# Optimization experiments

Hardware: AMD Instinct MI355X
Metric: run time of the kernel (lower is better)

## Reference

```python
import jax, jax.numpy as jnp
import numpy as np

D_MODEL = 1024
N_HEADS = 16
D_K = D_MODEL // N_HEADS
MAX_LEN = 2048
B, T = 2, 2048


def setup_inputs() -> dict:
    key = jax.random.key(0)
    ks = jax.random.split(key, 10)
    s = 1.0 / np.sqrt(D_MODEL)
    inp = {
        "x": jax.random.normal(ks[0], (B, T, D_MODEL), dtype=jnp.float32),
        "WQ": jax.random.uniform(ks[1], (D_MODEL, D_MODEL), minval=-s, maxval=s, dtype=jnp.float32),
        "bQ": jax.random.uniform(ks[2], (D_MODEL,), minval=-s, maxval=s, dtype=jnp.float32),
        "WK": jax.random.uniform(ks[3], (D_MODEL, D_MODEL), minval=-s, maxval=s, dtype=jnp.float32),
        "bK": jax.random.uniform(ks[4], (D_MODEL,), minval=-s, maxval=s, dtype=jnp.float32),
        "WV": jax.random.uniform(ks[5], (D_MODEL, D_MODEL), minval=-s, maxval=s, dtype=jnp.float32),
        "bV": jax.random.uniform(ks[6], (D_MODEL,), minval=-s, maxval=s, dtype=jnp.float32),
        "WO": jax.random.uniform(ks[7], (D_MODEL, D_MODEL), minval=-s, maxval=s, dtype=jnp.float32),
        "bO": jax.random.uniform(ks[8], (D_MODEL,), minval=-s, maxval=s, dtype=jnp.float32),
        "rel_pos_table": jax.random.normal(ks[9], (2 * MAX_LEN - 1, N_HEADS), dtype=jnp.float32),
    }
    return inp


def reference(x, WQ, bQ, WK, bK, WV, bV, WO, bO, rel_pos_table):
    b, t, d = x.shape
    # torch Linear: y = x @ W^T + b
    q = (x @ WQ.T + bQ).reshape(b, t, N_HEADS, D_K).transpose(0, 2, 1, 3)  # [B,H,T,dk]
    k = (x @ WK.T + bK).reshape(b, t, N_HEADS, D_K).transpose(0, 2, 1, 3)
    v = (x @ WV.T + bV).reshape(b, t, N_HEADS, D_K).transpose(0, 2, 1, 3)

    scores = jnp.einsum("bhqd,bhkd->bhqk", q, k) / jnp.sqrt(jnp.float32(D_K))

    pos = jnp.arange(t)
    rel = pos[:, None] - pos[None, :] + (MAX_LEN - 1)
    rel = jnp.clip(rel, 0, 2 * MAX_LEN - 2)
    rel_bias = rel_pos_table[rel]                  # [T,T,H]
    scores = scores + rel_bias.transpose(2, 0, 1)[None]  # [1,H,T,T]

    causal = pos[None, :] <= pos[:, None]          # [T,T] lower-triangular
    scores = jnp.where(causal[None, None], scores, -jnp.inf)

    attn = jax.nn.softmax(scores, axis=-1)
    out = jnp.einsum("bhqk,bhkd->bhqd", attn, v)   # [B,H,T,dk]
    out = out.transpose(0, 2, 1, 3).reshape(b, t, d)
    return out @ WO.T + bO
```

## Files before the change

### kernel.cpp

```cpp
#include <hip/hip_runtime.h>
#include <hip/hip_bf16.h>

typedef __attribute__((ext_vector_type(8))) short bf16x8;
typedef __attribute__((ext_vector_type(4))) float f32x4;
typedef __attribute__((ext_vector_type(16))) float f32x16;

#define MFMA16(a, b, c) __builtin_amdgcn_mfma_f32_16x16x32_bf16(a, b, c, 0, 0, 0)
#define MFMA32(a, b, c) __builtin_amdgcn_mfma_f32_32x32x16_bf16(a, b, c, 0, 0, 0)

__device__ inline ushort f2b(float f) {
  union { float f; unsigned u; } v; v.f = f;
  unsigned u = v.u;
  u += 0x7fffu + ((u >> 16) & 1u);
  return (ushort)(u >> 16);
}

__device__ inline unsigned cvtpk(float lo, float hi) {
  unsigned r;
  asm("v_cvt_pk_bf16_f32 %0, %1, %2" : "=v"(r) : "v"(lo), "v"(hi));
  return r;
}

__device__ inline void plswap(unsigned& a, unsigned& b) {
  asm("v_permlane32_swap_b32 %0, %1" : "+v"(a), "+v"(b));
}

__global__ void cast_k(const float* __restrict__ in, ushort* __restrict__ out, int n) {
  int i = (blockIdx.x * blockDim.x + threadIdx.x) * 4;
  const int stride = gridDim.x * blockDim.x * 4;
  for (; i < n; i += stride) {
    float4 v = *reinterpret_cast<const float4*>(in + i);
    ushort4 o;
    o.x = f2b(v.x); o.y = f2b(v.y); o.z = f2b(v.z); o.w = f2b(v.w);
    *reinterpret_cast<ushort4*>(out + i) = o;
  }
}

__global__ void cast_w(const float* __restrict__ wq, const float* __restrict__ wk,
                       const float* __restrict__ wv, const float* __restrict__ wo,
                       ushort* __restrict__ wcat, ushort* __restrict__ wob) {
  const int i = (blockIdx.x * 256 + threadIdx.x) * 4;
  const int which = i >> 20, off = i & 1048575;
  const float* src = (which == 0) ? wq : (which == 1) ? wk : (which == 2) ? wv : wo;
  float4 v = *reinterpret_cast<const float4*>(src + off);
  ushort4 o;
  o.x = f2b(v.x); o.y = f2b(v.y); o.z = f2b(v.z); o.w = f2b(v.w);
  if (which < 3) *reinterpret_cast<ushort4*>(wcat + i) = o;
  else           *reinterpret_cast<ushort4*>(wob + off) = o;
}

__global__ void prep_rel(const float* __restrict__ relT, float* __restrict__ relvT) {
  const int t = blockIdx.x * 256 + threadIdx.x;
  if (t >= 16 * 4095) return;
  const int h = t / 4095, d = t - h * 4095;
  relvT[t] = relT[(size_t)d * 16 + h] * 1.4426950408889634f;
}

__global__ __launch_bounds__(256, 4)
void repack_kv(const ushort* __restrict__ Kg, const ushort* __restrict__ VTg,
               ushort* __restrict__ Kf, ushort* __restrict__ Vf) {
  const int blk = blockIdx.x;
  const int bh = blk >> 5, t64 = blk & 31;
  const int tid = threadIdx.x;
  const int w = tid >> 6, lane = tid & 63;
  const int li = lane & 31, hi = lane >> 5;
  const size_t dstbase = (size_t)blk * 4096 + lane * 8;
  const int half = w & 1;
  if (w < 2) {
#pragma unroll
    for (int c = 0; c < 4; ++c) {
      bf16x8 v = *reinterpret_cast<const bf16x8*>(
          Kg + ((size_t)(bh * 2048 + t64 * 64 + half * 32 + li)) * 64 + c * 16 + hi * 8);
      *reinterpret_cast<bf16x8*>(Kf + dstbase + (half * 4 + c) * 512) = v;
    }
  } else {
#pragma unroll
    for (int c = 0; c < 4; ++c) {
      bf16x8 v = *reinterpret_cast<const bf16x8*>(
          VTg + ((size_t)(bh * 64 + half * 32 + li)) * 2048 + t64 * 64 + c * 16 + hi * 8);
      *reinterpret_cast<bf16x8*>(Vf + dstbase + (half * 4 + c) * 512) = v;
    }
  }
}

template <int MODE>
__global__ __launch_bounds__(256, 3)
void gemm_bt(const ushort* __restrict__ A, const ushort* __restrict__ B,
             const float* __restrict__ b0, const float* __restrict__ b1,
             const float* __restrict__ b2,
             float* __restrict__ outF, ushort* __restrict__ Qg,
             ushort* __restrict__ Kg, ushort* __restrict__ VTg, int N) {
  __shared__ __align__(16) ushort As[128][32];
  __shared__ __align__(16) ushort Bs[128][32];
  const int tid = threadIdx.x;
  const int m0 = blockIdx.y * 128, n0 = blockIdx.x * 128;
  const int wid = tid >> 6, lane = tid & 63, g = lane >> 4, li = lane & 15;
  const int wr = (wid >> 1) * 64, wc = (wid & 1) * 64;
  const int srow = lane >> 2, scol = (lane & 3) * 8;
  const ushort* gA0 = A + (size_t)(m0 + wid * 32 + srow) * 1024 + scol;
  const ushort* gB0 = B + (size_t)(n0 + wid * 32 + srow) * 1024 + scol;
  ushort* lA0 = &As[wid * 32][0];
  ushort* lA1 = &As[wid * 32 + 16][0];
  ushort* lB0 = &Bs[wid * 32][0];
  ushort* lB1 = &Bs[wid * 32 + 16][0];
  f32x4 acc[4][4] = {};
  for (int k0 = 0; k0 < 1024; k0 += 32) {
    __builtin_amdgcn_global_load_lds((const __attribute__((address_space(1))) void*)(gA0 + k0),
                                     (__attribute__((address_space(3))) void*)lA0, 16, 0, 0);
    __builtin_amdgcn_global_load_lds((const __attribute__((address_space(1))) void*)(gA0 + 16 * 1024 + k0),
                                     (__attribute__((address_space(3))) void*)lA1, 16, 0, 0);
    __builtin_amdgcn_global_load_lds((const __attribute__((address_space(1))) void*)(gB0 + k0),
                                     (__attribute__((address_space(3))) void*)lB0, 16, 0, 0);
    __builtin_amdgcn_global_load_lds((const __attribute__((address_space(1))) void*)(gB0 + 16 * 1024 + k0),
                                     (__attribute__((address_space(3))) void*)lB1, 16, 0, 0);
    __syncthreads();
    bf16x8 af[4], bfm[4];
#pragma unroll
    for (int i = 0; i < 4; ++i) {
      af[i]  = *reinterpret_cast<const bf16x8*>(&As[wr + i * 16 + li][g * 8]);
      bfm[i] = *reinterpret_cast<const bf16x8*>(&Bs[wc + i * 16 + li][g * 8]);
    }
#pragma unroll
    for (int mi = 0; mi < 4; ++mi)
#pragma unroll
      for (int ni = 0; ni < 4; ++ni)
        acc[mi][ni] = MFMA16(af[mi], bfm[ni], acc[mi][ni]);
    __syncthreads();
  }
#pragma unroll
  for (int mi = 0; mi < 4; ++mi) {
#pragma unroll
    for (int ni = 0; ni < 4; ++ni) {
      const int col = n0 + wc + ni * 16 + li;
      if (MODE == 0) {
#pragma unroll
        for (int r = 0; r < 4; ++r) {
          const int row = m0 + wr + mi * 16 + 4 * g + r;
          outF[(size_t)row * N + col] = acc[mi][ni][r] + b0[col];
        }
      } else {
        const int which = col >> 10, c = col & 1023;
        const int hh = c >> 6, dk = c & 63;
        const float* bias = (which == 0) ? b0 : ((which == 1) ? b1 : b2);
        const float bcol = bias[c];
        const int row0 = m0 + wr + mi * 16 + 4 * g;
        const int bb = row0 >> 11, t0 = row0 & 2047;
        const size_t bhi = (size_t)(bb * 16 + hh);
        if (which == 2) {
          ushort4 o;
          o.x = f2b(acc[mi][ni][0] + bcol);
          o.y = f2b(acc[mi][ni][1] + bcol);
          o.z = f2b(acc[mi][ni][2] + bcol);
          o.w = f2b(acc[mi][ni][3] + bcol);
          *reinterpret_cast<ushort4*>(VTg + (bhi * 64 + dk) * 2048 + t0) = o;
        } else {
          ushort* dst = ((which == 0) ? Qg : Kg) + (bhi * 2048 + t0) * 64 + dk;
#pragma unroll
          for (int r = 0; r < 4; ++r)
            dst[(size_t)r * 64] = f2b(acc[mi][ni][r] + bcol);
        }
      }
    }
  }
}

__device__ __forceinline__ void attn_phase(
    const int qt, const int wid, const int lane, const int li, const int hi,
    const int h, const int bb,
    const ushort* __restrict__ Qb, const ushort* __restrict__ Kfb,
    const ushort* __restrict__ Vfb, const float* relv,
    float Obuf[3][64][33], float lbuf[3][64], ushort* __restrict__ Oa) {
  const int q = qt * 32 + li;
  bf16x8 qf[4];
#pragma unroll
  for (int c = 0; c < 4; ++c)
    qf[c] = *reinterpret_cast<const bf16x8*>(Qb + (size_t)q * 64 + c * 16 + hi * 8);
  f32x16 O[2] = {};
  float lacc[4] = {0.f, 0.f, 0.f, 0.f};
  const int nkt = (qt >> 1) + 1;
  const int nt = (wid < nkt) ? ((nkt - 1 - wid) >> 2) + 1 : 0;
  const int mask_kb = (nkt - 1) * 64;
  const float C1 = 0.18033688f;
  for (int i = 0; i < nt; ++i) {
    const int kb = wid * 64 + i * 256;
    const ushort* Kt = Kfb + (size_t)(kb >> 6) * 4096 + lane * 8;
    const ushort* Vt = Vfb + (size_t)(kb >> 6) * 4096 + lane * 8;
    bf16x8 Kr[8], Vr[8];
#pragma unroll
    for (int j = 0; j < 8; ++j)
      Kr[j] = *reinterpret_cast<const bf16x8*>(Kt + j * 512);
#pragma unroll
    for (int j = 0; j < 8; ++j)
      Vr[j] = *reinterpret_cast<const bf16x8*>(Vt + j * 512);
    __builtin_amdgcn_sched_barrier(0);
    f32x16 S0 = {}, S1 = {};
#pragma unroll
    for (int c = 0; c < 4; ++c) S0 = MFMA32(Kr[c], qf[c], S0);
#pragma unroll
    for (int c = 0; c < 4; ++c) S1 = MFMA32(Kr[4 + c], qf[c], S1);
    const int dqb = q - kb - 4 * hi;
    const float* rl = relv + (dqb - 63);
    if (kb != mask_kb) {
#pragma unroll
      for (int r = 0; r < 16; ++r) {
        const int off0 = (r & 3) + 8 * (r >> 2);
        const float p0 = __builtin_amdgcn_exp2f(fmaf(S0[r], C1, rl[63 - off0]));
        const float p1 = __builtin_amdgcn_exp2f(fmaf(S1[r], C1, rl[31 - off0]));
        S0[r] = p0; S1[r] = p1;
        lacc[r & 3] += p0 + p1;
      }
    } else {
#pragma unroll
      for (int r = 0; r < 16; ++r) {
        const int off0 = (r & 3) + 8 * (r >> 2);
        const int d0 = dqb - off0, d1 = d0 - 32;
        float p0 = __builtin_amdgcn_exp2f(fmaf(S0[r], C1, relv[d0 & 2047]));
        float p1 = __builtin_amdgcn_exp2f(fmaf(S1[r], C1, relv[d1 & 2047]));
        p0 = (d0 >= 0) ? p0 : 0.f;
        p1 = (d1 >= 0) ? p1 : 0.f;
        S0[r] = p0; S1[r] = p1;
        lacc[r & 3] += p0 + p1;
      }
    }
    unsigned U0[4][2], U1[4][2];
#pragma unroll
    for (int rg = 0; rg < 4; ++rg) {
      U0[rg][0] = cvtpk(S0[4 * rg + 0], S0[4 * rg + 1]);
      U0[rg][1] = cvtpk(S0[4 * rg + 2], S0[4 * rg + 3]);
      U1[rg][0] = cvtpk(S1[4 * rg + 0], S1[4 * rg + 1]);
      U1[rg][1] = cvtpk(S1[4 * rg + 2], S1[4 * rg + 3]);
    }
#pragma unroll
    for (int c = 0; c < 4; ++c) {
      const int c0 = c & 1;
      unsigned x0 = (c < 2) ? U0[2 * c0][0] : U1[2 * c0][0];
      unsigned y0 = (c < 2) ? U0[2 * c0 + 1][0] : U1[2 * c0 + 1][0];
      unsigned x1 = (c < 2) ? U0[2 * c0][1] : U1[2 * c0][1];
      unsigned y1 = (c < 2) ? U0[2 * c0 + 1][1] : U1[2 * c0 + 1][1];
      plswap(x0, y0);
      plswap(x1, y1);
      union { unsigned u[4]; bf16x8 v; } P;
      P.u[0] = x0; P.u[1] = x1; P.u[2] = y0; P.u[3] = y1;
#pragma unroll
      for (int db = 0; db < 2; ++db)
        O[db] = MFMA32(Vr[db * 4 + c], P.v, O[db]);
    }
  }
  __syncthreads();
  if (wid) {
    float* ob = &Obuf[wid - 1][lane][0];
#pragma unroll
    for (int db = 0; db < 2; ++db)
#pragma unroll
      for (int r = 0; r < 16; ++r)
        ob[db * 16 + r] = O[db][r];
    lbuf[wid - 1][lane] = lacc[0] + lacc[1] + lacc[2] + lacc[3];
  }
  __syncthreads();
  if (wid == 0) {
    float lh = lacc[0] + lacc[1] + lacc[2] + lacc[3];
#pragma unroll
    for (int w = 0; w < 3; ++w) {
      lh += lbuf[w][lane];
      const float* ob = &Obuf[w][lane][0];
#pragma unroll
      for (int db = 0; db < 2; ++db)
#pragma unroll
        for (int r = 0; r < 16; ++r)
          O[db][r] += ob[db * 16 + r];
    }
    unsigned xa = __float_as_uint(lh), xb2 = xa;
    plswap(xa, xb2);
    const float linv = 1.f / (__uint_as_float(xa) + __uint_as_float(xb2));
    ushort* orow = Oa + ((size_t)(bb * 2048 + q)) * 1024 + h * 64;
#pragma unroll
    for (int db = 0; db < 2; ++db)
#pragma unroll
      for (int rg = 0; rg < 4; ++rg) {
        ushort4 o;
        o.x = f2b(O[db][4 * rg + 0] * linv);
        o.y = f2b(O[db][4 * rg + 1] * linv);
        o.z = f2b(O[db][4 * rg + 2] * linv);
        o.w = f2b(O[db][4 * rg + 3] * linv);
        *reinterpret_cast<ushort4*>(orow + db * 32 + 8 * rg + 4 * hi) = o;
      }
  }
}

__global__ __launch_bounds__(256, 2)
void attn_k(const ushort* __restrict__ Qg, const ushort* __restrict__ Kf,
            const ushort* __restrict__ Vf, const float* __restrict__ relvT,
            ushort* __restrict__ Oa) {
  __shared__ float relv[2048];
  __shared__ float Obuf[3][64][33];
  __shared__ float lbuf[3][64];
  const int f = blockIdx.x;
  const int bh = (f & 7) * 4 + (f >> 8);
  const int qp = (f >> 3) & 31;
  const int h = bh & 15, bb = bh >> 4;
  {
    const float* src = relvT + h * 4095 + 2047;
    for (int i = threadIdx.x; i < 2048; i += 256) relv[i] = src[i];
  }
  __syncthreads();
  const int wid = threadIdx.x >> 6, lane = threadIdx.x & 63;
  const int li = lane & 31, hi = lane >> 5;
  const ushort* Qb  = Qg + (size_t)bh * (2048 * 64);
  const ushort* Kfb = Kf + (size_t)bh * (32 * 4096);
  const ushort* Vfb = Vf + (size_t)bh * (32 * 4096);
  attn_phase(qp,      wid, lane, li, hi, h, bb, Qb, Kfb, Vfb, relv, Obuf, lbuf, Oa);
  attn_phase(63 - qp, wid, lane, li, hi, h, bb, Qb, Kfb, Vfb, relv, Obuf, lbuf, Oa);
}

extern "C" void kernel_launch(void* const* d_in, const int* in_sizes, int n_in,
                              void* d_out, int out_size, void* d_ws, size_t ws_size,
                              hipStream_t stream) {
  const float* x    = (const float*)d_in[0];
  const float* WQ   = (const float*)d_in[1];
  const float* bQ   = (const float*)d_in[2];
  const float* WK   = (const float*)d_in[3];
  const float* bK   = (const float*)d_in[4];
  const float* WV   = (const float*)d_in[5];
  const float* bV   = (const float*)d_in[6];
  const float* WO   = (const float*)d_in[7];
  const float* bO   = (const float*)d_in[8];
  const float* relT = (const float*)d_in[9];
  float* out = (float*)d_out;

  if (ws_size < (size_t)48 * 1024 * 1024) return;

  char* ws = (char*)d_ws;
  const size_t MB = 1024 * 1024;
  ushort* xb    = (ushort*)(ws);
  ushort* Kf    = (ushort*)(ws);
  ushort* Wcat  = (ushort*)(ws + 8 * MB);
  float*  relvT = (float*)(ws + 8 * MB);
  ushort* WOb   = (ushort*)(ws + 14 * MB);
  ushort* Qg    = (ushort*)(ws + 16 * MB);
  ushort* Kg    = (ushort*)(ws + 24 * MB);
  ushort* VTg   = (ushort*)(ws + 32 * MB);
  ushort* Oa    = (ushort*)(ws + 32 * MB);
  ushort* Vf    = (ushort*)(ws + 40 * MB);

  cast_k<<<1024, 256, 0, stream>>>(x, xb, 4096 * 1024);
  cast_w<<<4096, 256, 0, stream>>>(WQ, WK, WV, WO, Wcat, WOb);

  gemm_bt<1><<<dim3(24, 32), 256, 0, stream>>>(xb, Wcat, bQ, bK, bV,
                                               nullptr, Qg, Kg, VTg, 3072);
  prep_rel<<<256, 256, 0, stream>>>(relT, relvT);
  repack_kv<<<1024, 256, 0, stream>>>(Kg, VTg, Kf, Vf);
  attn_k<<<1024, 256, 0, stream>>>(Qg, Kf, Vf, relvT, Oa);
  gemm_bt<0><<<dim3(8, 32), 256, 0, stream>>>(Oa, WOb, bO, nullptr, nullptr,
                                              out, nullptr, nullptr, nullptr, 1024);
}
```

Baseline: 122.8 us.

## Double-buffer K loads in attention loop and widen GEMM K-tile to 64

The attention inner loop now prefetches the next K tile into an alternate register buffer while the current tile's QK MFMAs and softmax run. V loads are issued after the score MFMAs so their latency overlaps the exponent work. Separately, the projection GEMM stages a 64-wide K slice per LDS round instead of 32, which halves the barrier count. The cost is more registers (a second K buffer) and twice the LDS per GEMM block, which may reduce occupancy.

```diff
diff --git a/kernel.cpp b/kernel.cpp
--- a/kernel.cpp
+++ b/kernel.cpp
@@ -90,41 +90,40 @@
              const float* __restrict__ b2,
              float* __restrict__ outF, ushort* __restrict__ Qg,
              ushort* __restrict__ Kg, ushort* __restrict__ VTg, int N) {
-  __shared__ __align__(16) ushort As[128][32];
-  __shared__ __align__(16) ushort Bs[128][32];
+  __shared__ __align__(16) ushort As[128][64];
+  __shared__ __align__(16) ushort Bs[128][64];
   const int tid = threadIdx.x;
   const int m0 = blockIdx.y * 128, n0 = blockIdx.x * 128;
   const int wid = tid >> 6, lane = tid & 63, g = lane >> 4, li = lane & 15;
   const int wr = (wid >> 1) * 64, wc = (wid & 1) * 64;
-  const int srow = lane >> 2, scol = (lane & 3) * 8;
-  const ushort* gA0 = A + (size_t)(m0 + wid * 32 + srow) * 1024 + scol;
-  const ushort* gB0 = B + (size_t)(n0 + wid * 32 + srow) * 1024 + scol;
-  ushort* lA0 = &As[wid * 32][0];
-  ushort* lA1 = &As[wid * 32 + 16][0];
-  ushort* lB0 = &Bs[wid * 32][0];
-  ushort* lB1 = &Bs[wid * 32 + 16][0];
+  const int srow0 = (lane >> 3), scol = (lane & 7) * 8;
   f32x4 acc[4][4] = {};
-  for (int k0 = 0; k0 < 1024; k0 += 32) {
-    __builtin_amdgcn_global_load_lds((const __attribute__((address_space(1))) void*)(gA0 + k0),
-                                     (__attribute__((address_space(3))) void*)lA0, 16, 0, 0);
-    __builtin_amdgcn_global_load_lds((const __attribute__((address_space(1))) void*)(gA0 + 16 * 1024 + k0),
-                                     (__attribute__((address_space(3))) void*)lA1, 16, 0, 0);
-    __builtin_amdgcn_global_load_lds((const __attribute__((address_space(1))) void*)(gB0 + k0),
-                                     (__attribute__((address_space(3))) void*)lB0, 16, 0, 0);
-    __builtin_amdgcn_global_load_lds((const __attribute__((address_space(1))) void*)(gB0 + 16 * 1024 + k0),
-                                     (__attribute__((address_space(3))) void*)lB1, 16, 0, 0);
+  for (int k0 = 0; k0 < 1024; k0 += 64) {
+#pragma unroll
+    for (int it = 0; it < 4; ++it) {
+      const int rb = (wid * 4 + it) * 8;
+      __builtin_amdgcn_global_load_lds(
+          (const __attribute__((address_space(1))) void*)(A + (size_t)(m0 + rb + srow0) * 1024 + k0 + scol),
+          (__attribute__((address_space(3))) void*)(&As[0][0] + (wid * 4 + it) * 512), 16, 0, 0);
+      __builtin_amdgcn_global_load_lds(
+          (const __attribute__((address_space(1))) void*)(B + (size_t)(n0 + rb + srow0) * 1024 + k0 + scol),
+          (__attribute__((address_space(3))) void*)(&Bs[0][0] + (wid * 4 + it) * 512), 16, 0, 0);
+    }
     __syncthreads();
-    bf16x8 af[4], bfm[4];
-#pragma unroll
-    for (int i = 0; i < 4; ++i) {
-      af[i]  = *reinterpret_cast<const bf16x8*>(&As[wr + i * 16 + li][g * 8]);
-      bfm[i] = *reinterpret_cast<const bf16x8*>(&Bs[wc + i * 16 + li][g * 8]);
-    }
-#pragma unroll
-    for (int mi = 0; mi < 4; ++mi)
-#pragma unroll
-      for (int ni = 0; ni < 4; ++ni)
-        acc[mi][ni] = MFMA16(af[mi], bfm[ni], acc[mi][ni]);
+#pragma unroll
+    for (int kk = 0; kk < 64; kk += 32) {
+      bf16x8 af[4], bfm[4];
+#pragma unroll
+      for (int i = 0; i < 4; ++i) {
+        af[i]  = *reinterpret_cast<const bf16x8*>(&As[wr + i * 16 + li][kk + g * 8]);
+        bfm[i] = *reinterpret_cast<const bf16x8*>(&Bs[wc + i * 16 + li][kk + g * 8]);
+      }
+#pragma unroll
+      for (int mi = 0; mi < 4; ++mi)
+#pragma unroll
+        for (int ni = 0; ni < 4; ++ni)
+          acc[mi][ni] = MFMA16(af[mi], bfm[ni], acc[mi][ni]);
+    }
     __syncthreads();
   }
 #pragma unroll
@@ -164,6 +163,77 @@
   }
 }
 
+#define ATTN_BODY(KC, KN)                                                        \
+  do {                                                                           \
+    const int kbn_ = (i + 1 < nt) ? (kb + 256) : kb;                             \
+    __builtin_amdgcn_sched_barrier(0);                                           \
+    f32x16 S0 = {}, S1 = {};                                                     \
+    _Pragma("unroll")                                                            \
+    for (int c = 0; c < 4; ++c) S0 = MFMA32(KC[c], qf[c], S0);                   \
+    _Pragma("unroll")                                                            \
+    for (int c = 0; c < 4; ++c) S1 = MFMA32(KC[4 + c], qf[c], S1);               \
+    __builtin_amdgcn_sched_barrier(0);                                           \
+    {                                                                            \
+      const ushort* Vt_ = Vfb + (size_t)(kb >> 6) * 4096 + lane * 8;             \
+      _Pragma("unroll")                                                          \
+      for (int j = 0; j < 8; ++j)                                                \
+        Vr[j] = *reinterpret_cast<const bf16x8*>(Vt_ + j * 512);                 \
+      const ushort* Kt_ = Kfb + (size_t)(kbn_ >> 6) * 4096 + lane * 8;           \
+      _Pragma("unroll")                                                          \
+      for (int j = 0; j < 8; ++j)                                                \
+        KN[j] = *reinterpret_cast<const bf16x8*>(Kt_ + j * 512);                 \
+    }                                                                            \
+    __builtin_amdgcn_sched_barrier(0);                                           \
+    const int dqb = q - kb - 4 * hi;                                             \
+    const float* rl = relv + (dqb - 63);                                         \
+    if (kb != mask_kb) {                                                         \
+      _Pragma("unroll")                                                          \
+      for (int r = 0; r < 16; ++r) {                                             \
+        const int off0 = (r & 3) + 8 * (r >> 2);                                 \
+        const float p0 = __builtin_amdgcn_exp2f(fmaf(S0[r], C1, rl[63 - off0])); \
+        const float p1 = __builtin_amdgcn_exp2f(fmaf(S1[r], C1, rl[31 - off0])); \
+        S0[r] = p0; S1[r] = p1;                                                  \
+        lacc[r & 3] += p0 + p1;                                                  \
+      }                                                                          \
+    } else {                                                                     \
+      _Pragma("unroll")                                                          \
+      for (int r = 0; r < 16; ++r) {                                             \
+        const int off0 = (r & 3) + 8 * (r >> 2);                                 \
+        const int d0 = dqb - off0, d1 = d0 - 32;                                 \
+        float p0 = __builtin_amdgcn_exp2f(fmaf(S0[r], C1, relv[d0 & 2047]));     \
+        float p1 = __builtin_amdgcn_exp2f(fmaf(S1[r], C1, relv[d1 & 2047]));     \
+        p0 = (d0 >= 0) ? p0 : 0.f;                                               \
+        p1 = (d1 >= 0) ? p1 : 0.f;                                               \
+        S0[r] = p0; S1[r] = p1;                                                  \
+        lacc[r & 3] += p0 + p1;                                                  \
+      }                                                                          \
+    }                                                                            \
+    unsigned U0[4][2], U1[4][2];                                                 \
+    _Pragma("unroll")                                                            \
+    for (int rg = 0; rg < 4; ++rg) {                                             \
+      U0[rg][0] = cvtpk(S0[4 * rg + 0], S0[4 * rg + 1]);                         \
+      U0[rg][1] = cvtpk(S0[4 * rg + 2], S0[4 * rg + 3]);                         \
+      U1[rg][0] = cvtpk(S1[4 * rg + 0], S1[4 * rg + 1]);                         \
+      U1[rg][1] = cvtpk(S1[4 * rg + 2], S1[4 * rg + 3]);                         \
+    }                                                                            \
+    _Pragma("unroll")                                                            \
+    for (int c = 0; c < 4; ++c) {                                                \
+      const int c0 = c & 1;                                                      \
+      unsigned x0 = (c < 2) ? U0[2 * c0][0] : U1[2 * c0][0];                     \
+      unsigned y0 = (c < 2) ? U0[2 * c0 + 1][0] : U1[2 * c0 + 1][0];             \
+      unsigned x1 = (c < 2) ? U0[2 * c0][1] : U1[2 * c0][1];                     \
+      unsigned y1 = (c < 2) ? U0[2 * c0 + 1][1] : U1[2 * c0 + 1][1];             \
+      plswap(x0, y0);                                                            \
+      plswap(x1, y1);                                                            \
+      union { unsigned u[4]; bf16x8 v; } P;                                      \
+      P.u[0] = x0; P.u[1] = x1; P.u[2] = y0; P.u[3] = y1;                        \
+      O[0] = MFMA32(Vr[c], P.v, O[0]);                                           \
+      O[1] = MFMA32(Vr[4 + c], P.v, O[1]);                                       \
+    }                                                                            \
+    kb += 256;                                                                   \
+    ++i;                                                                         \
+  } while (0)
+
 __device__ __forceinline__ void attn_phase(
     const int qt, const int wid, const int lane, const int li, const int hi,
     const int h, const int bb,
@@ -181,69 +251,20 @@
   const int nt = (wid < nkt) ? ((nkt - 1 - wid) >> 2) + 1 : 0;
   const int mask_kb = (nkt - 1) * 64;
   const float C1 = 0.18033688f;
-  for (int i = 0; i < nt; ++i) {
-    const int kb = wid * 64 + i * 256;
-    const ushort* Kt = Kfb + (size_t)(kb >> 6) * 4096 + lane * 8;
-    const ushort* Vt = Vfb + (size_t)(kb >> 6) * 4096 + lane * 8;
-    bf16x8 Kr[8], Vr[8];
-#pragma unroll
-    for (int j = 0; j < 8; ++j)
-      Kr[j] = *reinterpret_cast<const bf16x8*>(Kt + j * 512);
-#pragma unroll
-    for (int j = 0; j < 8; ++j)
-      Vr[j] = *reinterpret_cast<const bf16x8*>(Vt + j * 512);
-    __builtin_amdgcn_sched_barrier(0);
-    f32x16 S0 = {}, S1 = {};
-#pragma unroll
-    for (int c = 0; c < 4; ++c) S0 = MFMA32(Kr[c], qf[c], S0);
-#pragma unroll
-    for (int c = 0; c < 4; ++c) S1 = MFMA32(Kr[4 + c], qf[c], S1);
-    const int dqb = q - kb - 4 * hi;
-    const float* rl = relv + (dqb - 63);
-    if (kb != mask_kb) {
-#pragma unroll
-      for (int r = 0; r < 16; ++r) {
-        const int off0 = (r & 3) + 8 * (r >> 2);
-        const float p0 = __builtin_amdgcn_exp2f(fmaf(S0[r], C1, rl[63 - off0]));
-        const float p1 = __builtin_amdgcn_exp2f(fmaf(S1[r], C1, rl[31 - off0]));
-        S0[r] = p0; S1[r] = p1;
-        lacc[r & 3] += p0 + p1;
-      }
-    } else {
-#pragma unroll
-      for (int r = 0; r < 16; ++r) {
-        const int off0 = (r & 3) + 8 * (r >> 2);
-        const int d0 = dqb - off0, d1 = d0 - 32;
-        float p0 = __builtin_amdgcn_exp2f(fmaf(S0[r], C1, relv[d0 & 2047]));
-        float p1 = __builtin_amdgcn_exp2f(fmaf(S1[r], C1, relv[d1 & 2047]));
-        p0 = (d0 >= 0) ? p0 : 0.f;
-        p1 = (d1 >= 0) ? p1 : 0.f;
-        S0[r] = p0; S1[r] = p1;
-        lacc[r & 3] += p0 + p1;
-      }
-    }
-    unsigned U0[4][2], U1[4][2];
-#pragma unroll
-    for (int rg = 0; rg < 4; ++rg) {
-      U0[rg][0] = cvtpk(S0[4 * rg + 0], S0[4 * rg + 1]);
-      U0[rg][1] = cvtpk(S0[4 * rg + 2], S0[4 * rg + 3]);
-      U1[rg][0] = cvtpk(S1[4 * rg + 0], S1[4 * rg + 1]);
-      U1[rg][1] = cvtpk(S1[4 * rg + 2], S1[4 * rg + 3]);
-    }
-#pragma unroll
-    for (int c = 0; c < 4; ++c) {
-      const int c0 = c & 1;
-      unsigned x0 = (c < 2) ? U0[2 * c0][0] : U1[2 * c0][0];
-      unsigned y0 = (c < 2) ? U0[2 * c0 + 1][0] : U1[2 * c0 + 1][0];
-      unsigned x1 = (c < 2) ? U0[2 * c0][1] : U1[2 * c0][1];
-      unsigned y1 = (c < 2) ? U0[2 * c0 + 1][1] : U1[2 * c0 + 1][1];
-      plswap(x0, y0);
-      plswap(x1, y1);
-      union { unsigned u[4]; bf16x8 v; } P;
-      P.u[0] = x0; P.u[1] = x1; P.u[2] = y0; P.u[3] = y1;
-#pragma unroll
-      for (int db = 0; db < 2; ++db)
-        O[db] = MFMA32(Vr[db * 4 + c], P.v, O[db]);
+  if (nt > 0) {
+    int i = 0, kb = wid * 64;
+    bf16x8 KrA[8], KrB[8], Vr[8];
+    {
+      const ushort* Kt0 = Kfb + (size_t)(kb >> 6) * 4096 + lane * 8;
+#pragma unroll
+      for (int j = 0; j < 8; ++j)
+        KrA[j] = *reinterpret_cast<const bf16x8*>(Kt0 + j * 512);
+    }
+    while (true) {
+      ATTN_BODY(KrA, KrB);
+      if (i >= nt) break;
+      ATTN_BODY(KrB, KrA);
+      if (i >= nt) break;
     }
   }
   __syncthreads();
@@ -286,6 +307,7 @@
       }
   }
 }
+#undef ATTN_BODY
 
 __global__ __launch_bounds__(256, 2)
 void attn_k(const ushort* __restrict__ Qg, const ushort* __restrict__ Kf,
```

Result: no change. 123.8 us (+0.9%).
